# Kernel tuning notes

Hardware: AMD Instinct MI355X
Metric: run time of the kernel (lower is better)

The kernel has to match this reference:

```python
import jax, jax.numpy as jnp
import numpy as np

D_MODEL = 1024
D_Q = 1024
D_K = 1024
D_V = 1024
B, S = 4, 2048


def setup_inputs() -> dict:
    key = jax.random.key(0)
    kx, kq, kk, kv = jax.random.split(key, 4)
    # torch Linear(in, out) weight is [out, in]; y = x @ W.T. Use kaiming-ish scale.
    sc = 1.0 / np.sqrt(D_MODEL)
    x = jax.random.normal(kx, (B, S, D_MODEL), dtype=jnp.float32)
    Wq = jax.random.normal(kq, (D_Q, D_MODEL), dtype=jnp.float32) * sc
    Wk = jax.random.normal(kk, (D_K, D_MODEL), dtype=jnp.float32) * sc
    Wv = jax.random.normal(kv, (D_V, D_MODEL), dtype=jnp.float32) * sc
    return {"x": x, "Wq": Wq, "Wk": Wk, "Wv": Wv}


def reference(x, Wq, Wk, Wv):
    d_k = Wk.shape[0]
    q = jnp.einsum('bsd,qd->bsq', x, Wq)  # [B,S,d_q]
    k = jnp.einsum('bsd,kd->bsk', x, Wk)  # [B,S,d_k]
    v = jnp.einsum('bsd,vd->bsv', x, Wv)  # [B,S,d_v]
    scores = jnp.einsum('bqd,bkd->bqk', q, k) / jnp.sqrt(jnp.float32(d_k))
    seq = scores.shape[-1]
    causal = jnp.tril(jnp.ones((seq, seq), dtype=bool))  # True = keep
    scores = jnp.where(causal[None, :, :], scores, -jnp.inf)
    probs = jax.nn.softmax(scores, axis=-1)
    return jnp.einsum('bqk,bkv->bqv', probs, v)
```

## Files before the change

### kernel.cpp

```cpp
#include <hip/hip_runtime.h>
#include <hip/hip_bf16.h>
#include <stdint.h>

typedef __attribute__((ext_vector_type(8))) short short8;
typedef __attribute__((ext_vector_type(4))) float floatx4;

typedef const __attribute__((address_space(1))) void* gvp;
typedef __attribute__((address_space(3))) void* lvp;

__device__ __forceinline__ unsigned short f2bf(float f) {
    unsigned u = __float_as_uint(f);
    u += 0x7fffu + ((u >> 16) & 1u);
    return (unsigned short)(u >> 16);
}

#define BAR()   do { asm volatile("" ::: "memory"); __builtin_amdgcn_s_barrier(); asm volatile("" ::: "memory"); } while (0)
#define WAITL() do { asm volatile("s_waitcnt lgkmcnt(0)" ::: "memory"); __builtin_amdgcn_sched_barrier(0); } while (0)
#define WAITV4() asm volatile("s_waitcnt vmcnt(4)" ::: "memory")
#define WAITV0() asm volatile("s_waitcnt vmcnt(0)" ::: "memory")

__global__ __launch_bounds__(256)
void cvt_all(const float* __restrict__ x, const float* __restrict__ wq,
             const float* __restrict__ wk, const float* __restrict__ wv,
             unsigned short* __restrict__ Xb, unsigned short* __restrict__ Wb) {
    const long NX = 8192l * 1024 / 4;
    const long NW = 1024l * 1024 / 4;
    long i = (long)blockIdx.x * blockDim.x + threadIdx.x;
    long stride = (long)gridDim.x * blockDim.x;
    for (long idx = i; idx < NX + 3 * NW; idx += stride) {
        const float* in; unsigned short* out; long off;
        if (idx < NX) { in = x; out = Xb; off = idx; }
        else {
            long r = idx - NX;
            int sel = (int)(r >> 18);
            off = r & (NW - 1);
            in = (sel == 0) ? wq : (sel == 1) ? wk : wv;
            out = Wb + (long)sel * NW * 4;
        }
        float4 v = reinterpret_cast<const float4*>(in)[off];
        uint2 o;
        o.x = (unsigned)f2bf(v.x) | ((unsigned)f2bf(v.y) << 16);
        o.y = (unsigned)f2bf(v.z) | ((unsigned)f2bf(v.w) << 16);
        reinterpret_cast<uint2*>(out)[off] = o;
    }
}

__device__ __forceinline__ void stage_half(char* slot, const unsigned short* src,
                                           int ld, int k0, int tid) {
    #pragma unroll
    for (int r = 0; r < 2; ++r) {
        const int c = r * 512 + tid;
        const int row = c >> 3;
        const int cs = ((c & 7) * 16) ^ ((row & 7) << 4);
        const char* g = reinterpret_cast<const char*>(src + (long)row * ld + k0) + cs;
        __builtin_amdgcn_global_load_lds((gvp)g,
            (lvp)(slot + r * 8192 + (tid >> 6) * 1024), 16, 0, 0);
    }
}

__device__ __forceinline__ void load_a4(short8 a_[4][2], const char* slot, int mh,
                                        int fr, int csw0, int csw1) {
    #pragma unroll
    for (int i = 0; i < 4; ++i) {
        const int rb = (mh * 64 + i * 16 + fr) * 128;
        a_[i][0] = *reinterpret_cast<const short8*>(slot + rb + csw0);
        a_[i][1] = *reinterpret_cast<const short8*>(slot + rb + csw1);
    }
}

__device__ __forceinline__ void load_b2(short8 b_[2][2], const char* slot, int rbase,
                                        int nh, int fr, int csw0, int csw1) {
    #pragma unroll
    for (int j = 0; j < 2; ++j) {
        const int rb = (rbase + nh * 32 + j * 16 + fr) * 128;
        b_[j][0] = *reinterpret_cast<const short8*>(slot + rb + csw0);
        b_[j][1] = *reinterpret_cast<const short8*>(slot + rb + csw1);
    }
}

__device__ __forceinline__ void mfma16(floatx4 acc[8][4], short8 a_[4][2],
                                       short8 b_[2][2], int mh, int nh) {
    __builtin_amdgcn_s_setprio(1);
    #pragma unroll
    for (int i = 0; i < 4; ++i)
        #pragma unroll
        for (int j = 0; j < 2; ++j) {
            acc[mh*4+i][nh*2+j] = __builtin_amdgcn_mfma_f32_16x16x32_bf16(
                a_[i][0], b_[j][0], acc[mh*4+i][nh*2+j], 0, 0, 0);
            acc[mh*4+i][nh*2+j] = __builtin_amdgcn_mfma_f32_16x16x32_bf16(
                a_[i][1], b_[j][1], acc[mh*4+i][nh*2+j], 0, 0, 0);
        }
    __builtin_amdgcn_s_setprio(0);
}

template<typename CT, int MODE>
__global__ __launch_bounds__(512, 2)
void gemm8p(const unsigned short* __restrict__ A, const unsigned short* __restrict__ B,
            CT* __restrict__ C, unsigned short* __restrict__ Vt,
            int K, int lda, int ldb, int ldc,
            long sA, long sB, long sC, int nwg)
{
    const int gx = gridDim.x, gy = gridDim.y;
    int flat = (blockIdx.z * gy + blockIdx.y) * gx + blockIdx.x;
    {
        int xcd = flat & 7, lid = flat >> 3;
        int q = nwg >> 3, r = nwg & 7;
        flat = (xcd < r ? xcd * (q + 1) : r * (q + 1) + (xcd - r) * q) + lid;
    }
    const int bx = flat % gx;
    const int t2 = flat / gx;
    const int by = t2 % gy;
    const int bz = t2 / gy;
    if (MODE == 1 && bx > by) return;

    A += (long)bz * sA + (long)by * 256 * lda;
    B += (long)bz * sB + (long)bx * 256 * ldb;
    C += (long)bz * sC;

    __shared__ __align__(16) char lds[8 * 16384];
    #define SLOT(db, op, half) (lds + ((((db) << 1 | (op)) << 1 | (half)) * 16384))

    const int tid  = threadIdx.x;
    const int lane = tid & 63;
    const int wid  = tid >> 6;
    const int wm = wid >> 2;
    const int wn = wid & 3;
    const int bh = wn >> 1;
    const int brbase = (wn & 1) * 64;
    const int fr = lane & 15;
    const int csw0 = ((lane >> 4) * 16) ^ ((fr & 7) << 4);
    const int csw1 = (64 + (lane >> 4) * 16) ^ ((fr & 7) << 4);

    const unsigned short* Ah[2] = { A, A + 128ll * lda };
    const unsigned short* Bh[2] = { B, B + 128ll * ldb };

    const int NT = K >> 6;
    const int NI = NT >> 1;

    floatx4 acc[8][4] = {};
    short8 a_[4][2];
    short8 b_[2][2][2];

    stage_half(SLOT(0,1,0), Bh[0], ldb, 0, tid);
    stage_half(SLOT(0,1,1), Bh[1], ldb, 0, tid);
    stage_half(SLOT(0,0,0), Ah[0], lda, 0, tid);
    stage_half(SLOT(0,0,1), Ah[1], lda, 0, tid);
    stage_half(SLOT(1,1,0), Bh[0], ldb, 64, tid);
    stage_half(SLOT(1,1,1), Bh[1], ldb, 64, tid);
    WAITV4();
    BAR();

    for (int I = 0; I < NI; ++I) {
        const int kA1 = min(2*I + 1, NT - 1) * 64;
        const int kT2 = min(2*I + 2, NT - 1) * 64;
        const int kB3 = min(2*I + 3, NT - 1) * 64;

        load_a4(a_, SLOT(0,0,wm), 0, fr, csw0, csw1);
        load_b2(b_[0], SLOT(0,1,bh), brbase, 0, fr, csw0, csw1);
        stage_half(SLOT(1,0,0), Ah[0], lda, kA1, tid);
        BAR(); WAITL();
        mfma16(acc, a_, b_[0], 0, 0);
        BAR();

        load_b2(b_[1], SLOT(0,1,bh), brbase, 1, fr, csw0, csw1);
        stage_half(SLOT(1,0,1), Ah[1], lda, kA1, tid);
        BAR(); WAITL();
        mfma16(acc, a_, b_[1], 0, 1);
        BAR();

        load_a4(a_, SLOT(0,0,wm), 1, fr, csw0, csw1);
        stage_half(SLOT(0,1,0), Bh[0], ldb, kT2, tid);
        BAR(); WAITL();
        mfma16(acc, a_, b_[1], 1, 1);
        BAR();

        stage_half(SLOT(0,1,1), Bh[1], ldb, kT2, tid);
        BAR(); WAITL();
        mfma16(acc, a_, b_[0], 1, 0);
        WAITV4();
        BAR();

        load_a4(a_, SLOT(1,0,wm), 0, fr, csw0, csw1);
        load_b2(b_[0], SLOT(1,1,bh), brbase, 0, fr, csw0, csw1);
        stage_half(SLOT(0,0,0), Ah[0], lda, kT2, tid);
        BAR(); WAITL();
        mfma16(acc, a_, b_[0], 0, 0);
        BAR();

        load_b2(b_[1], SLOT(1,1,bh), brbase, 1, fr, csw0, csw1);
        stage_half(SLOT(0,0,1), Ah[1], lda, kT2, tid);
        BAR(); WAITL();
        mfma16(acc, a_, b_[1], 0, 1);
        BAR();

        load_a4(a_, SLOT(1,0,wm), 1, fr, csw0, csw1);
        stage_half(SLOT(1,1,0), Bh[0], ldb, kB3, tid);
        BAR(); WAITL();
        mfma16(acc, a_, b_[1], 1, 1);
        BAR();

        stage_half(SLOT(1,1,1), Bh[1], ldb, kB3, tid);
        BAR(); WAITL();
        mfma16(acc, a_, b_[0], 1, 0);
        WAITV4();
        BAR();
    }

    if (MODE == 0 && bz == 2) {
        WAITV0();
        BAR();
        char* T = lds;
        #pragma unroll
        for (int i = 0; i < 8; ++i)
            #pragma unroll
            for (int j = 0; j < 4; ++j) {
                const int n = wn * 64 + j * 16 + fr;
                const int m = wm * 128 + ((lane >> 4) << 2) + i * 16;
                uint2 pk;
                pk.x = (unsigned)f2bf(acc[i][j][0]) | ((unsigned)f2bf(acc[i][j][1]) << 16);
                pk.y = (unsigned)f2bf(acc[i][j][2]) | ((unsigned)f2bf(acc[i][j][3]) << 16);
                *reinterpret_cast<uint2*>(T + n * 512 + ((m * 2) ^ ((n & 7) << 4))) = pk;
            }
        __syncthreads();
        const int b  = by >> 3;
        const int s0 = (by & 7) * 256;
        #pragma unroll
        for (int c = 0; c < 16; ++c) {
            const int idx = c * 512 + tid;
            const int n = idx >> 5, k = idx & 31;
            uint4 v = *reinterpret_cast<const uint4*>(T + n * 512 + ((k * 16) ^ ((n & 7) << 4)));
            *reinterpret_cast<uint4*>(Vt + (long)b * (1024 * 2048)
                + (long)(bx * 256 + n) * 2048 + s0 + k * 8) = v;
        }
        return;
    }

    const int cr0 = by * 256 + wm * 128 + (lane >> 4) * 4;
    const int cc0 = bx * 256 + wn * 64 + (lane & 15);
    #pragma unroll
    for (int i = 0; i < 8; ++i)
        #pragma unroll
        for (int j = 0; j < 4; ++j)
            #pragma unroll
            for (int r = 0; r < 4; ++r) {
                long idx = (long)(cr0 + i * 16 + r) * ldc + (cc0 + j * 16);
                float v = acc[i][j][r];
                if constexpr (sizeof(CT) == 4) C[idx] = v;
                else                           C[idx] = (CT)f2bf(v);
            }
    #undef SLOT
}

template<typename CT, int MODE>
__global__ __launch_bounds__(256, 3)
void gemm_bt(const unsigned short* __restrict__ A, const unsigned short* __restrict__ B,
             CT* __restrict__ C, int K, int lda, int ldb, int ldc,
             long sA, long sB, long sC, int nwg)
{
    const int gx = gridDim.x, gy = gridDim.y;
    int flat = (blockIdx.z * gy + blockIdx.y) * gx + blockIdx.x;
    {
        int xcd = flat & 7, lid = flat >> 3;
        int q = nwg >> 3, r = nwg & 7;
        flat = (xcd < r ? xcd * (q + 1) : r * (q + 1) + (xcd - r) * q) + lid;
    }
    int bx = flat % gx;
    int t2 = flat / gx;
    int by = t2 % gy;
    const int bz = t2 / gy;
    if (MODE == 2) {
        by = ((by & 1) << 3) | ((by & 2) << 1) | ((by & 4) >> 1) | ((by & 8) >> 3);
    }

    A += (long)bz * sA; B += (long)bz * sB; C += (long)bz * sC;
    const int kend = (MODE == 2) ? min(K, (by + 1) * 128) : K;

    __shared__ unsigned short As[128 * 64];
    __shared__ unsigned short Bs[128 * 64];

    const int tid  = threadIdx.x;
    const int lane = tid & 63;
    const int wid  = tid >> 6;
    const int m0 = by * 128, n0 = bx * 128;
    const int wm = (wid >> 1) * 64, wn = (wid & 1) * 64;
    const int frow = lane & 15;
    const int fk   = (lane >> 4) * 8;

    const int srow = lane >> 3;
    const int scolb = (lane & 7) * 16;

    floatx4 acc[4][4] = {};

    for (int k0 = 0; k0 < kend; k0 += 64) {
        __syncthreads();
        #pragma unroll
        for (int i = 0; i < 4; ++i) {
            const int c = wid * 4 + i;
            const int row = c * 8 + srow;
            const char* ga = reinterpret_cast<const char*>(A + (long)(m0 + row) * lda + k0) + scolb;
            __builtin_amdgcn_global_load_lds((gvp)ga,
                (lvp)(reinterpret_cast<char*>(As) + c * 1024), 16, 0, 0);
            const char* gb = reinterpret_cast<const char*>(B + (long)(n0 + row) * ldb + k0) + scolb;
            __builtin_amdgcn_global_load_lds((gvp)gb,
                (lvp)(reinterpret_cast<char*>(Bs) + c * 1024), 16, 0, 0);
        }
        __syncthreads();
        #pragma unroll
        for (int ks = 0; ks < 2; ++ks) {
            short8 af[4], bf[4];
            #pragma unroll
            for (int i = 0; i < 4; ++i) {
                const int ar = wm + i * 16 + frow;
                af[i] = *reinterpret_cast<const short8*>(
                    reinterpret_cast<const char*>(As) + ar * 128 + (ks * 32 + fk) * 2);
                const int br = wn + i * 16 + frow;
                bf[i] = *reinterpret_cast<const short8*>(
                    reinterpret_cast<const char*>(Bs) + br * 128 + (ks * 32 + fk) * 2);
            }
            #pragma unroll
            for (int i = 0; i < 4; ++i)
                #pragma unroll
                for (int j = 0; j < 4; ++j)
                    acc[i][j] = __builtin_amdgcn_mfma_f32_16x16x32_bf16(af[i], bf[j], acc[i][j], 0, 0, 0);
        }
    }

    const int cr0 = m0 + wm + (lane >> 4) * 4;
    const int cc0 = n0 + wn + (lane & 15);
    #pragma unroll
    for (int i = 0; i < 4; ++i)
        #pragma unroll
        for (int j = 0; j < 4; ++j)
            #pragma unroll
            for (int r = 0; r < 4; ++r) {
                long idx = (long)(cr0 + i * 16 + r) * ldc + (cc0 + j * 16);
                float v = acc[i][j][r];
                if constexpr (sizeof(CT) == 4) C[idx] = v;
                else                           C[idx] = (CT)f2bf(v);
            }
}

__global__ __launch_bounds__(256)
void softmax_causal(float* __restrict__ Sc) {
    const int q = blockIdx.x;
    const int b = blockIdx.y;
    float* row = Sc + ((long)b * 2048 + q) * 2048;
    const int t = threadIdx.x;
    const int lane = t & 63, wid = t >> 6;
    const int kend = (q | 127) + 1;

    float vals[8];
    float mx = -INFINITY;
    #pragma unroll
    for (int i = 0; i < 2; ++i) {
        const int c0 = i * 1024 + t * 4;
        if (c0 <= q) {
            float4 v = *reinterpret_cast<const float4*>(row + c0);
            float tmp[4] = {v.x, v.y, v.z, v.w};
            #pragma unroll
            for (int j = 0; j < 4; ++j) {
                float val = (c0 + j <= q) ? tmp[j] * 0.03125f : -INFINITY;
                vals[i * 4 + j] = val;
                mx = fmaxf(mx, val);
            }
        } else {
            vals[i*4+0] = vals[i*4+1] = vals[i*4+2] = vals[i*4+3] = -INFINITY;
        }
    }
    #pragma unroll
    for (int o = 32; o > 0; o >>= 1) mx = fmaxf(mx, __shfl_xor(mx, o));
    __shared__ float rmax[4], rsum[4];
    if (lane == 0) rmax[wid] = mx;
    __syncthreads();
    mx = fmaxf(fmaxf(rmax[0], rmax[1]), fmaxf(rmax[2], rmax[3]));

    float s = 0.f;
    #pragma unroll
    for (int k = 0; k < 8; ++k) {
        float e = __expf(vals[k] - mx);
        vals[k] = e;
        s += e;
    }
    #pragma unroll
    for (int o = 32; o > 0; o >>= 1) s += __shfl_xor(s, o);
    if (lane == 0) rsum[wid] = s;
    __syncthreads();
    s = rsum[0] + rsum[1] + rsum[2] + rsum[3];
    const float inv = 1.f / s;

    unsigned short* orow = reinterpret_cast<unsigned short*>(row);
    #pragma unroll
    for (int i = 0; i < 2; ++i) {
        const int c0 = i * 1024 + t * 4;
        if (c0 < kend) {
            uint2 o;
            o.x = (unsigned)f2bf(vals[i*4+0] * inv) | ((unsigned)f2bf(vals[i*4+1] * inv) << 16);
            o.y = (unsigned)f2bf(vals[i*4+2] * inv) | ((unsigned)f2bf(vals[i*4+3] * inv) << 16);
            *reinterpret_cast<uint2*>(orow + c0) = o;
        }
    }
}

extern "C" void kernel_launch(void* const* d_in, const int* in_sizes, int n_in,
                              void* d_out, int out_size, void* d_ws, size_t ws_size,
                              hipStream_t stream) {
    const float* x  = (const float*)d_in[0];
    const float* Wq = (const float*)d_in[1];
    const float* Wk = (const float*)d_in[2];
    const float* Wv = (const float*)d_in[3];
    float* out = (float*)d_out;

    char* w = (char*)d_ws;
    unsigned short* Xb = (unsigned short*)(w);
    unsigned short* Wb = (unsigned short*)(w + (16ll << 20));
    unsigned short* Qb = (unsigned short*)(w + (22ll << 20));
    unsigned short* Kb = (unsigned short*)(w + (38ll << 20));
    unsigned short* Vt = (unsigned short*)(w + (70ll << 20));
    float* Sc = (float*)(w + (86ll << 20));

    dim3 blk(256);
    cvt_all<<<2816, blk, 0, stream>>>(x, Wq, Wk, Wv, Xb, Wb);

    gemm8p<unsigned short, 0><<<dim3(4, 32, 3), dim3(512), 0, stream>>>(
        Xb, Wb, Qb, Vt, 1024, 1024, 1024, 1024,
        0, 1024ll * 1024, 8192ll * 1024, 4 * 32 * 3);

    gemm8p<float, 1><<<dim3(8, 8, 4), dim3(512), 0, stream>>>(
        Qb, Kb, Sc, nullptr, 1024, 1024, 1024, 2048,
        2048ll * 1024, 2048ll * 1024, 2048ll * 2048, 8 * 8 * 4);

    softmax_causal<<<dim3(2048, 4), blk, 0, stream>>>(Sc);

    gemm_bt<float, 2><<<dim3(8, 16, 4), blk, 0, stream>>>(
        (const unsigned short*)Sc, Vt, out, 2048, 4096, 2048, 1024,
        2048ll * 4096, 1024ll * 2048, 2048ll * 1024, 8 * 16 * 4);
}
```

Measured before the change: 166.9 us.

## Fold Wq and Wk into one Gram matrix to replace the K projection

Scores are computed as X·(Wq^T Wk /sqrt(d))·X^T. A small 1024x1024 GEMM builds G from transposed Wq and Wk with the scale folded in, so the projection GEMM only produces Y = X·G and V, and the score GEMM reads X directly instead of K. This removes one third of the projection work and the K buffer. The scale multiply moves out of the softmax. It adds a weight transpose inside the conversion kernel and a small extra GEMM launch, and rounding G to bf16 changes numerics slightly.

```diff
diff --git a/kernel.cpp b/kernel.cpp
--- a/kernel.cpp
+++ b/kernel.cpp
@@ -22,26 +22,46 @@
 __global__ __launch_bounds__(256)
 void cvt_all(const float* __restrict__ x, const float* __restrict__ wq,
              const float* __restrict__ wk, const float* __restrict__ wv,
-             unsigned short* __restrict__ Xb, unsigned short* __restrict__ Wb) {
-    const long NX = 8192l * 1024 / 4;
-    const long NW = 1024l * 1024 / 4;
-    long i = (long)blockIdx.x * blockDim.x + threadIdx.x;
-    long stride = (long)gridDim.x * blockDim.x;
-    for (long idx = i; idx < NX + 3 * NW; idx += stride) {
-        const float* in; unsigned short* out; long off;
-        if (idx < NX) { in = x; out = Xb; off = idx; }
-        else {
-            long r = idx - NX;
-            int sel = (int)(r >> 18);
-            off = r & (NW - 1);
-            in = (sel == 0) ? wq : (sel == 1) ? wk : wv;
-            out = Wb + (long)sel * NW * 4;
-        }
-        float4 v = reinterpret_cast<const float4*>(in)[off];
-        uint2 o;
-        o.x = (unsigned)f2bf(v.x) | ((unsigned)f2bf(v.y) << 16);
-        o.y = (unsigned)f2bf(v.z) | ((unsigned)f2bf(v.w) << 16);
-        reinterpret_cast<uint2*>(out)[off] = o;
+             unsigned short* __restrict__ Xb, unsigned short* __restrict__ WqT,
+             unsigned short* __restrict__ WkT, unsigned short* __restrict__ Wvb) {
+    const int b = blockIdx.x, t = threadIdx.x;
+    if (b < 2304) {
+        const float* in; unsigned short* out; long base;
+        if (b < 2048) { in = x;  out = Xb;  base = (long)b * 1024; }
+        else          { in = wv; out = Wvb; base = (long)(b - 2048) * 1024; }
+        #pragma unroll
+        for (int k = 0; k < 4; ++k) {
+            long idx = base + k * 256 + t;
+            float4 v = reinterpret_cast<const float4*>(in)[idx];
+            uint2 o;
+            o.x = (unsigned)f2bf(v.x) | ((unsigned)f2bf(v.y) << 16);
+            o.y = (unsigned)f2bf(v.z) | ((unsigned)f2bf(v.w) << 16);
+            reinterpret_cast<uint2*>(out)[idx] = o;
+        }
+    } else {
+        const int bb = b - 2304;
+        const float* in = (bb < 256) ? wq : wk;
+        unsigned short* out = (bb < 256) ? WqT : WkT;
+        const int tile = bb & 255;
+        const int e0 = (tile >> 4) * 64, d0 = (tile & 15) * 64;
+        __shared__ unsigned short ldsT[64][68];
+        const int r = t >> 4, cq = t & 15;
+        #pragma unroll
+        for (int p = 0; p < 4; ++p) {
+            const int e = p * 16 + r;
+            float4 v = *reinterpret_cast<const float4*>(in + (long)(e0 + e) * 1024 + d0 + cq * 4);
+            ldsT[cq*4+0][e] = f2bf(v.x);
+            ldsT[cq*4+1][e] = f2bf(v.y);
+            ldsT[cq*4+2][e] = f2bf(v.z);
+            ldsT[cq*4+3][e] = f2bf(v.w);
+        }
+        __syncthreads();
+        #pragma unroll
+        for (int p = 0; p < 4; ++p) {
+            const int d = p * 16 + r;
+            ushort4 o = *reinterpret_cast<const ushort4*>(&ldsT[d][cq * 4]);
+            *reinterpret_cast<ushort4*>(out + (long)(d0 + d) * 1024 + e0 + cq * 4) = o;
+        }
     }
 }
 
@@ -95,8 +115,8 @@
 
 template<typename CT, int MODE>
 __global__ __launch_bounds__(512, 2)
-void gemm8p(const unsigned short* __restrict__ A, const unsigned short* __restrict__ B,
-            CT* __restrict__ C, unsigned short* __restrict__ Vt,
+void gemm8p(const unsigned short* __restrict__ A, const unsigned short* B,
+            const unsigned short* B1, CT* __restrict__ C, unsigned short* __restrict__ Vt,
             int K, int lda, int ldb, int ldc,
             long sA, long sB, long sC, int nwg)
 {
@@ -107,11 +127,19 @@
         int q = nwg >> 3, r = nwg & 7;
         flat = (xcd < r ? xcd * (q + 1) : r * (q + 1) + (xcd - r) * q) + lid;
     }
-    const int bx = flat % gx;
-    const int t2 = flat / gx;
-    const int by = t2 % gy;
-    const int bz = t2 / gy;
-    if (MODE == 1 && bx > by) return;
+    int bx, by, bz = 0;
+    bool isV = false;
+    if (MODE == 1) {
+        bx = flat % gx;
+        int t2 = flat / gx;
+        by = t2 % gy;
+        bz = t2 / gy;
+        if (bx > by) return;
+    } else {
+        if (flat >= 128) { isV = true; flat -= 128; B = B1; }
+        by = flat >> 2;
+        bx = flat & 3;
+    }
 
     A += (long)bz * sA + (long)by * 256 * lda;
     B += (long)bz * sB + (long)bx * 256 * ldb;
@@ -206,7 +234,7 @@
         BAR();
     }
 
-    if (MODE == 0 && bz == 2) {
+    if (MODE == 3 && isV) {
         WAITV0();
         BAR();
         char* T = lds;
@@ -255,7 +283,7 @@
 __global__ __launch_bounds__(256, 3)
 void gemm_bt(const unsigned short* __restrict__ A, const unsigned short* __restrict__ B,
              CT* __restrict__ C, int K, int lda, int ldb, int ldc,
-             long sA, long sB, long sC, int nwg)
+             long sA, long sB, long sC, int nwg, float csc)
 {
     const int gx = gridDim.x, gy = gridDim.y;
     int flat = (blockIdx.z * gy + blockIdx.y) * gx + blockIdx.x;
@@ -334,7 +362,7 @@
             #pragma unroll
             for (int r = 0; r < 4; ++r) {
                 long idx = (long)(cr0 + i * 16 + r) * ldc + (cc0 + j * 16);
-                float v = acc[i][j][r];
+                float v = acc[i][j][r] * csc;
                 if constexpr (sizeof(CT) == 4) C[idx] = v;
                 else                           C[idx] = (CT)f2bf(v);
             }
@@ -359,7 +387,7 @@
             float tmp[4] = {v.x, v.y, v.z, v.w};
             #pragma unroll
             for (int j = 0; j < 4; ++j) {
-                float val = (c0 + j <= q) ? tmp[j] * 0.03125f : -INFINITY;
+                float val = (c0 + j <= q) ? tmp[j] : -INFINITY;
                 vals[i * 4 + j] = val;
                 mx = fmaxf(mx, val);
             }
@@ -411,27 +439,32 @@
     float* out = (float*)d_out;
 
     char* w = (char*)d_ws;
-    unsigned short* Xb = (unsigned short*)(w);
-    unsigned short* Wb = (unsigned short*)(w + (16ll << 20));
-    unsigned short* Qb = (unsigned short*)(w + (22ll << 20));
-    unsigned short* Kb = (unsigned short*)(w + (38ll << 20));
-    unsigned short* Vt = (unsigned short*)(w + (70ll << 20));
+    unsigned short* Xb  = (unsigned short*)(w);
+    unsigned short* WqT = (unsigned short*)(w + (16ll << 20));
+    unsigned short* WkT = (unsigned short*)(w + (18ll << 20));
+    unsigned short* Wvb = (unsigned short*)(w + (20ll << 20));
+    unsigned short* Yb  = (unsigned short*)(w + (22ll << 20));
+    unsigned short* Gp  = (unsigned short*)(w + (38ll << 20));
+    unsigned short* Vt  = (unsigned short*)(w + (70ll << 20));
     float* Sc = (float*)(w + (86ll << 20));
 
     dim3 blk(256);
-    cvt_all<<<2816, blk, 0, stream>>>(x, Wq, Wk, Wv, Xb, Wb);
-
-    gemm8p<unsigned short, 0><<<dim3(4, 32, 3), dim3(512), 0, stream>>>(
-        Xb, Wb, Qb, Vt, 1024, 1024, 1024, 1024,
-        0, 1024ll * 1024, 8192ll * 1024, 4 * 32 * 3);
+    cvt_all<<<2816, blk, 0, stream>>>(x, Wq, Wk, Wv, Xb, WqT, WkT, Wvb);
+
+    gemm_bt<unsigned short, 0><<<dim3(8, 8, 1), blk, 0, stream>>>(
+        WkT, WqT, Gp, 1024, 1024, 1024, 1024, 0, 0, 0, 64, 0.03125f);
+
+    gemm8p<unsigned short, 3><<<dim3(256, 1, 1), dim3(512), 0, stream>>>(
+        Xb, Gp, Wvb, Yb, Vt, 1024, 1024, 1024, 1024,
+        0, 0, 0, 256);
 
     gemm8p<float, 1><<<dim3(8, 8, 4), dim3(512), 0, stream>>>(
-        Qb, Kb, Sc, nullptr, 1024, 1024, 1024, 2048,
-        2048ll * 1024, 2048ll * 1024, 2048ll * 2048, 8 * 8 * 4);
+        Yb, Xb, nullptr, Sc, nullptr, 1024, 1024, 1024, 2048,
+        2048ll * 1024, 2048ll * 1024, 2048ll * 2048, 256);
 
     softmax_causal<<<dim3(2048, 4), blk, 0, stream>>>(Sc);
 
     gemm_bt<float, 2><<<dim3(8, 16, 4), blk, 0, stream>>>(
         (const unsigned short*)Sc, Vt, out, 2048, 4096, 2048, 1024,
-        2048ll * 4096, 1024ll * 2048, 2048ll * 1024, 8 * 16 * 4);
-}
+        2048ll * 4096, 1024ll * 2048, 2048ll * 1024, 512, 1.0f);
+}
```

New measurement: 161.5 us. 1.03x faster.
